# Performance work log

Hardware: AMD Instinct MI355X
Metric: run time of the kernel (lower is better)

Reference implementation:

```python
import jax, jax.numpy as jnp
import numpy as np

B, C, N, M, K = 1, 64, 65536, 65536, 16
H, O = 64, 128  # mlp hidden, out_channels


def setup_inputs() -> dict:
    key = jax.random.key(0)
    ks = jax.random.split(key, 8)
    return {
        "x": jax.random.normal(ks[0], (B, C, N), dtype=jnp.float32),
        "pos": jax.random.normal(ks[1], (B, 3, N), dtype=jnp.float32),
        "support_points": jax.random.normal(ks[2], (B, 3, M), dtype=jnp.float32),
        "W1": jax.random.normal(ks[3], (H, C + 3), dtype=jnp.float32) * 0.05,
        "b1": jax.random.normal(ks[4], (H,), dtype=jnp.float32) * 0.05,
        "W2": jax.random.normal(ks[5], (O, H), dtype=jnp.float32) * 0.05,
        "b2": jax.random.normal(ks[6], (O,), dtype=jnp.float32) * 0.05,
        "indices": jax.random.randint(ks[7], (B, M, K), 0, N, dtype=jnp.int64),
    }


def _gather_points(t, indices):
    # t: [B, C, N], indices: [B, M, K] -> [B, C, M, K]
    b, c, n = t.shape
    m, k = indices.shape[1], indices.shape[2]
    idx = indices.reshape(b, 1, m * k)  # broadcasts over channel dim
    return jnp.take_along_axis(t, idx, axis=2).reshape(b, c, m, k)


def reference(x, pos, support_points, W1, b1, W2, b2, indices):
    # gather neighbor features and positions: [B, C, M, K], [B, 3, M, K]
    feats = _gather_points(x, indices)
    pts = _gather_points(pos, indices) - support_points[:, :, :, None]
    h = jnp.concatenate([feats, pts], axis=1)  # [B, C+3, M, K]
    # shared per-point MLP (1x1 Conv2d == channel contraction)
    h = jnp.einsum("oc,bcmk->bomk", W1, h) + b1[None, :, None, None]
    h = jax.nn.relu(h)
    h = jnp.einsum("oc,bcmk->bomk", W2, h) + b2[None, :, None, None]
    # max-pool over neighborhood K -> [B, O, M]
    return jnp.max(h, axis=3)
```

## Files before the change

### kernel.cpp

```cpp
#include <hip/hip_runtime.h>
#include <hip/hip_bf16.h>

#define NPTS 65536
#define MPTS 65536

typedef __attribute__((ext_vector_type(8))) short bf16x8;
typedef __attribute__((ext_vector_type(4))) float f32x4;

__device__ __forceinline__ float bflo(unsigned int u){ union{unsigned int i; float f;} v; v.i = u<<16; return v.f; }
__device__ __forceinline__ float bfhi(unsigned int u){ union{unsigned int i; float f;} v; v.i = u & 0xffff0000u; return v.f; }
__device__ __forceinline__ unsigned short f2bf(float f){
  union{float f; unsigned int i;} v; v.f=f;
  unsigned int r = v.i + 0x7fffu + ((v.i>>16)&1u);
  return (unsigned short)(r>>16);
}
__device__ __forceinline__ unsigned int pk2f(float a, float b){
  float2 tf; tf.x = a; tf.y = b;
  union { __hip_bfloat162 h; unsigned int u; } c;
  c.h = __float22bfloat162_rn(tf);
  return c.u;
}

#define MFMA32(a,b,c) __builtin_amdgcn_mfma_f32_16x16x32_bf16((a),(b),(c),0,0,0)

__global__ __launch_bounds__(256) void pack_u(
    const float* __restrict__ x,
    const float* __restrict__ pos,
    const float* __restrict__ W1,
    const float* __restrict__ b1,
    const float* __restrict__ W2,
    unsigned short* __restrict__ U,
    unsigned short* __restrict__ W2F) {
  const int t = threadIdx.x;
  if (blockIdx.x >= 1024) {
    const int gg = (blockIdx.x - 1024) * 256 + t;
    if (gg < 1024) {
      const int g = gg >> 6, lane = gg & 63;
      const int q = lane >> 4, lr = lane & 15;
      const int kt = g >> 3, ot = g & 7;
      #pragma unroll
      for (int j = 0; j < 4; ++j)
        *(unsigned int*)&W2F[gg*8 + 2*j] =
            pk2f(W2[(ot*16 + lr)*64 + kt*32 + q*8 + 2*j],
                 W2[(ot*16 + lr)*64 + kt*32 + q*8 + 2*j + 1]);
    }
    return;
  }
  const int lane = t & 63, w = t >> 6, quad = lane >> 4, lr = lane & 15;
  const int n = blockIdx.x * 64 + w * 16 + lr;

  bf16x8 wa[2][4], wt[4];
  #pragma unroll
  for (int kt = 0; kt < 2; ++kt)
    #pragma unroll
    for (int nt = 0; nt < 4; ++nt) {
      const float* r = W1 + (size_t)(nt*16 + lr)*67 + kt*32 + quad*8;
      const float4 a = *(const float4*)r;
      const float4 b = *(const float4*)(r + 4);
      union { unsigned int d[4]; bf16x8 v; } mk;
      mk.d[0] = pk2f(a.x, a.y); mk.d[1] = pk2f(a.z, a.w);
      mk.d[2] = pk2f(b.x, b.y); mk.d[3] = pk2f(b.z, b.w);
      wa[kt][nt] = mk.v;
    }
  #pragma unroll
  for (int nt = 0; nt < 4; ++nt) {
    union { unsigned int d[4]; bf16x8 v; } mk;
    mk.d[0] = 0u; mk.d[1] = 0u; mk.d[2] = 0u; mk.d[3] = 0u;
    if (quad == 0) {
      const float* r = W1 + (size_t)(nt*16 + lr)*67 + 64;
      mk.d[0] = pk2f(r[0], r[1]);
      mk.d[1] = (unsigned int)f2bf(r[2]);
    }
    wt[nt] = mk.v;
  }

  const f32x4 fz = {0.f, 0.f, 0.f, 0.f};
  f32x4 acc[4] = {fz, fz, fz, fz};
  #pragma unroll
  for (int kt = 0; kt < 2; ++kt) {
    const float* xc = x + (size_t)(kt*32 + quad*8) * NPTS + n;
    union { unsigned int d[4]; bf16x8 v; } mk;
    #pragma unroll
    for (int i = 0; i < 4; ++i)
      mk.d[i] = pk2f(xc[(size_t)(2*i) * NPTS], xc[(size_t)(2*i + 1) * NPTS]);
    #pragma unroll
    for (int nt = 0; nt < 4; ++nt)
      acc[nt] = MFMA32(wa[kt][nt], mk.v, acc[nt]);
  }
  {
    union { unsigned int d[4]; bf16x8 v; } mk;
    mk.d[0] = pk2f(pos[n], pos[NPTS + n]);
    mk.d[1] = (unsigned int)f2bf(pos[2*NPTS + n]);
    mk.d[2] = 0u; mk.d[3] = 0u;
    #pragma unroll
    for (int nt = 0; nt < 4; ++nt)
      acc[nt] = MFMA32(wt[nt], mk.v, acc[nt]);
  }
  #pragma unroll
  for (int nt = 0; nt < 4; ++nt) {
    const float4 bb = *(const float4*)(b1 + nt*16 + quad*4);
    uint2 d;
    d.x = pk2f(acc[nt][0] + bb.x, acc[nt][1] + bb.y);
    d.y = pk2f(acc[nt][2] + bb.z, acc[nt][3] + bb.w);
    *(uint2*)(U + (size_t)n * 64 + nt*16 + quad*4) = d;
  }
}

__global__ __launch_bounds__(256, 3) void pointnet_reg(
    const unsigned short* __restrict__ U,
    const float* __restrict__ sup,
    const float* __restrict__ W1,
    const unsigned short* __restrict__ W2F,
    const float* __restrict__ b2,
    const int* __restrict__ indices,
    float* __restrict__ out) {
  const int t = threadIdx.x;
  const int lane = t & 63, w = t >> 6, quad = lane >> 4, lr = lane & 15;
  const int wbase = blockIdx.x * 32 + w * 8;

  int idx[8];
  #pragma unroll
  for (int pt = 0; pt < 8; ++pt) idx[pt] = indices[(wbase + pt)*16 + lr];

  uint4 ur[8][2];
  #pragma unroll
  for (int pt = 0; pt < 8; ++pt)
    #pragma unroll
    for (int kt = 0; kt < 2; ++kt)
      ur[pt][kt] = *(const uint4*)(U + (size_t)idx[pt]*64 + kt*32 + quad*8);

  bf16x8 ah[8][2];
  #pragma unroll
  for (int kt = 0; kt < 2; ++kt) {
    float w1p[8][3];
    #pragma unroll
    for (int j = 0; j < 8; ++j) {
      const float* r = W1 + (size_t)(kt*32 + quad*8 + j)*67 + 64;
      w1p[j][0] = r[0]; w1p[j][1] = r[1]; w1p[j][2] = r[2];
    }
    #pragma unroll
    for (int pt = 0; pt < 8; ++pt) {
      const float s0 = sup[wbase + pt];
      const float s1 = sup[MPTS + wbase + pt];
      const float s2 = sup[2*MPTS + wbase + pt];
      const unsigned int uu[4] = {ur[pt][kt].x, ur[pt][kt].y, ur[pt][kt].z, ur[pt][kt].w};
      union { unsigned int d[4]; bf16x8 v; } mk;
      #pragma unroll
      for (int i = 0; i < 4; ++i) {
        const float vl = w1p[2*i][0]*s0 + w1p[2*i][1]*s1 + w1p[2*i][2]*s2;
        const float vh = w1p[2*i+1][0]*s0 + w1p[2*i+1][1]*s1 + w1p[2*i+1][2]*s2;
        const float hl = fmaxf(bflo(uu[i]) - vl, 0.f);
        const float hh = fmaxf(bfhi(uu[i]) - vh, 0.f);
        mk.d[i] = pk2f(hl, hh);
      }
      ah[pt][kt] = mk.v;
    }
  }

  const f32x4 fz = {0.f, 0.f, 0.f, 0.f};
  #pragma unroll
  for (int ot = 0; ot < 8; ++ot) {
    const bf16x8 wb0 = ((const bf16x8*)W2F)[(0*8 + ot)*64 + lane];
    const bf16x8 wb1 = ((const bf16x8*)W2F)[(1*8 + ot)*64 + lane];
    float vm[8];
    #pragma unroll
    for (int pt = 0; pt < 8; ++pt) {
      f32x4 a2 = MFMA32(ah[pt][0], wb0, fz);
      a2 = MFMA32(ah[pt][1], wb1, a2);
      float v = fmaxf(fmaxf(a2[0], a2[1]), fmaxf(a2[2], a2[3]));
      v = fmaxf(v, __shfl_xor(v, 16));
      v = fmaxf(v, __shfl_xor(v, 32));
      vm[pt] = v;
    }
    const int o = ot*16 + lr;
    const float bb = b2[o];
    const float va = (quad & 1) ? ((quad & 2) ? vm[3] : vm[1])
                                : ((quad & 2) ? vm[2] : vm[0]);
    const float vb = (quad & 1) ? ((quad & 2) ? vm[7] : vm[5])
                                : ((quad & 2) ? vm[6] : vm[4]);
    out[(size_t)o * MPTS + wbase + quad] = va + bb;
    out[(size_t)o * MPTS + wbase + 4 + quad] = vb + bb;
  }
}

__global__ __launch_bounds__(256) void pointnet_fallback(
    const float* __restrict__ x, const float* __restrict__ pos,
    const float* __restrict__ sup,
    const float* __restrict__ W1, const float* __restrict__ b1,
    const float* __restrict__ W2, const float* __restrict__ b2,
    const int* __restrict__ indices, float* __restrict__ out) {
  __shared__ float sfeat[16][68];
  __shared__ float shid[16][64];
  __shared__ float smax[4][128];
  __shared__ int sidx[16];
  const int t = threadIdx.x;
  const int m = blockIdx.x;
  if (t < 16) sidx[t] = indices[m*16 + t];
  const float sup0 = sup[m], sup1 = sup[MPTS + m], sup2 = sup[2*MPTS + m];
  __syncthreads();
  for (int u = t; u < 16*17; u += 256) {
    const int k = u / 17, c4 = (u - k*17) * 4;
    const int idx = sidx[k];
    float4 wv;
    if (c4 < 64) {
      wv.x = x[(size_t)(c4+0)*NPTS + idx]; wv.y = x[(size_t)(c4+1)*NPTS + idx];
      wv.z = x[(size_t)(c4+2)*NPTS + idx]; wv.w = x[(size_t)(c4+3)*NPTS + idx];
    } else {
      wv.x = pos[idx] - sup0; wv.y = pos[NPTS + idx] - sup1;
      wv.z = pos[2*NPTS + idx] - sup2; wv.w = 0.f;
    }
    *(float4*)&sfeat[k][c4] = wv;
  }
  const int h = t & 63, kg = t >> 6;
  float w1r[68];
  #pragma unroll
  for (int c = 0; c < 67; ++c) w1r[c] = W1[h*67 + c];
  w1r[67] = 0.f;
  const float bias1 = b1[h];
  __syncthreads();
  #pragma unroll
  for (int j = 0; j < 4; ++j) {
    const int k = kg*4 + j;
    float a = bias1;
    const float4* rr = (const float4*)sfeat[k];
    #pragma unroll
    for (int qq = 0; qq < 17; ++qq) {
      const float4 v = rr[qq];
      a += w1r[qq*4+0]*v.x + w1r[qq*4+1]*v.y + w1r[qq*4+2]*v.z + w1r[qq*4+3]*v.w;
    }
    shid[k][h] = fmaxf(a, 0.f);
  }
  const int ow = t & 63;
  float w2a[64], w2b[64];
  #pragma unroll
  for (int hh = 0; hh < 64; ++hh) { w2a[hh] = W2[ow*64 + hh]; w2b[hh] = W2[(ow+64)*64 + hh]; }
  __syncthreads();
  float mxa = -3.0e38f, mxb = -3.0e38f;
  #pragma unroll
  for (int j = 0; j < 4; ++j) {
    const int k = kg*4 + j;
    const float4* hr = (const float4*)shid[k];
    float pa = 0.f, pb = 0.f;
    #pragma unroll
    for (int qq = 0; qq < 16; ++qq) {
      const float4 v = hr[qq];
      pa += w2a[qq*4+0]*v.x + w2a[qq*4+1]*v.y + w2a[qq*4+2]*v.z + w2a[qq*4+3]*v.w;
      pb += w2b[qq*4+0]*v.x + w2b[qq*4+1]*v.y + w2b[qq*4+2]*v.z + w2b[qq*4+3]*v.w;
    }
    mxa = fmaxf(mxa, pa); mxb = fmaxf(mxb, pb);
  }
  smax[kg][ow] = mxa; smax[kg][64 + ow] = mxb;
  __syncthreads();
  if (t < 128) {
    out[(size_t)t * MPTS + m] =
        fmaxf(fmaxf(smax[0][t], smax[1][t]), fmaxf(smax[2][t], smax[3][t])) + b2[t];
  }
}

extern "C" void kernel_launch(void* const* d_in, const int* in_sizes, int n_in,
                              void* d_out, int out_size, void* d_ws, size_t ws_size,
                              hipStream_t stream) {
  const float* x   = (const float*)d_in[0];
  const float* pos = (const float*)d_in[1];
  const float* sup = (const float*)d_in[2];
  const float* W1  = (const float*)d_in[3];
  const float* b1  = (const float*)d_in[4];
  const float* W2  = (const float*)d_in[5];
  const float* b2  = (const float*)d_in[6];
  const int* indices = (const int*)d_in[7];
  float* out = (float*)d_out;

  const size_t U_BYTES   = (size_t)NPTS * 64 * 2;
  const size_t W2F_BYTES = 16 * 64 * 8 * 2;
  if (ws_size >= U_BYTES + W2F_BYTES) {
    unsigned short* U   = (unsigned short*)d_ws;
    unsigned short* W2F = (unsigned short*)((char*)d_ws + U_BYTES);
    pack_u<<<NPTS/64 + 4, 256, 0, stream>>>(x, pos, W1, b1, W2, U, W2F);
    pointnet_reg<<<MPTS/32, 256, 0, stream>>>(U, sup, W1, W2F, b2, indices, out);
  } else {
    pointnet_fallback<<<MPTS, 256, 0, stream>>>(x, pos, sup, W1, b1, W2, b2, indices, out);
  }
}
```

Baseline: 136.9 us.

## Precompute per-support W1·support term into fp32 table and subtract in main kernel

Adds a pre-pass inside the pack kernel that computes, for each support point, the 64-wide product of the position columns of W1 with the support coordinates, stored as fp32 V. A new main kernel loads this row per support point and subtracts it from the gathered bf16 first-layer pre-activations before ReLU. This avoids recomputing the support-point contribution of W1 in the main kernel. In exchange it writes and reads an extra 16 MB fp32 workspace.

```diff
diff --git a/kernel.cpp b/kernel.cpp
--- a/kernel.cpp
+++ b/kernel.cpp
@@ -26,12 +26,32 @@
 __global__ __launch_bounds__(256) void pack_u(
     const float* __restrict__ x,
     const float* __restrict__ pos,
+    const float* __restrict__ sup,
     const float* __restrict__ W1,
     const float* __restrict__ b1,
     const float* __restrict__ W2,
     unsigned short* __restrict__ U,
-    unsigned short* __restrict__ W2F) {
+    unsigned short* __restrict__ W2F,
+    float* __restrict__ V) {
   const int t = threadIdx.x;
+  if (blockIdx.x >= 1028) {
+    const int m = (blockIdx.x - 1028) * 256 + t;
+    const float s0 = sup[m], s1 = sup[MPTS + m], s2 = sup[2*MPTS + m];
+    #pragma unroll
+    for (int cg = 0; cg < 16; ++cg) {
+      const float* r0 = W1 + (size_t)(cg*4 + 0)*67 + 64;
+      const float* r1 = W1 + (size_t)(cg*4 + 1)*67 + 64;
+      const float* r2 = W1 + (size_t)(cg*4 + 2)*67 + 64;
+      const float* r3 = W1 + (size_t)(cg*4 + 3)*67 + 64;
+      float4 o;
+      o.x = r0[0]*s0 + r0[1]*s1 + r0[2]*s2;
+      o.y = r1[0]*s0 + r1[1]*s1 + r1[2]*s2;
+      o.z = r2[0]*s0 + r2[1]*s1 + r2[2]*s2;
+      o.w = r3[0]*s0 + r3[1]*s1 + r3[2]*s2;
+      *(float4*)(V + (size_t)m*64 + cg*4) = o;
+    }
+    return;
+  }
   if (blockIdx.x >= 1024) {
     const int gg = (blockIdx.x - 1024) * 256 + t;
     if (gg < 1024) {
@@ -103,6 +123,77 @@
     d.x = pk2f(acc[nt][0] + bb.x, acc[nt][1] + bb.y);
     d.y = pk2f(acc[nt][2] + bb.z, acc[nt][3] + bb.w);
     *(uint2*)(U + (size_t)n * 64 + nt*16 + quad*4) = d;
+  }
+}
+
+__global__ __launch_bounds__(256, 3) void pointnet_reg2(
+    const unsigned short* __restrict__ U,
+    const float* __restrict__ V,
+    const unsigned short* __restrict__ W2F,
+    const float* __restrict__ b2,
+    const int* __restrict__ indices,
+    float* __restrict__ out) {
+  const int t = threadIdx.x;
+  const int lane = t & 63, w = t >> 6, quad = lane >> 4, lr = lane & 15;
+  const int wbase = blockIdx.x * 32 + w * 8;
+
+  int idx[8];
+  #pragma unroll
+  for (int pt = 0; pt < 8; ++pt) idx[pt] = indices[(wbase + pt)*16 + lr];
+
+  uint4 ur[8][2];
+  #pragma unroll
+  for (int pt = 0; pt < 8; ++pt)
+    #pragma unroll
+    for (int kt = 0; kt < 2; ++kt)
+      ur[pt][kt] = *(const uint4*)(U + (size_t)idx[pt]*64 + kt*32 + quad*8);
+
+  bf16x8 ah[8][2];
+  #pragma unroll
+  for (int pt = 0; pt < 8; ++pt) {
+    const float* vr = V + (size_t)(wbase + pt)*64 + quad*8;
+    float vv[16];
+    *(float4*)&vv[0]  = *(const float4*)(vr);
+    *(float4*)&vv[4]  = *(const float4*)(vr + 4);
+    *(float4*)&vv[8]  = *(const float4*)(vr + 32);
+    *(float4*)&vv[12] = *(const float4*)(vr + 36);
+    #pragma unroll
+    for (int kt = 0; kt < 2; ++kt) {
+      const unsigned int uu[4] = {ur[pt][kt].x, ur[pt][kt].y, ur[pt][kt].z, ur[pt][kt].w};
+      union { unsigned int d[4]; bf16x8 v; } mk;
+      #pragma unroll
+      for (int i = 0; i < 4; ++i) {
+        const float lo = bflo(uu[i]) - vv[kt*8 + 2*i];
+        const float hi = bfhi(uu[i]) - vv[kt*8 + 2*i + 1];
+        mk.d[i] = pk2f(fmaxf(lo, 0.f), fmaxf(hi, 0.f));
+      }
+      ah[pt][kt] = mk.v;
+    }
+  }
+
+  const f32x4 fz = {0.f, 0.f, 0.f, 0.f};
+  #pragma unroll
+  for (int ot = 0; ot < 8; ++ot) {
+    const bf16x8 wb0 = ((const bf16x8*)W2F)[(0*8 + ot)*64 + lane];
+    const bf16x8 wb1 = ((const bf16x8*)W2F)[(1*8 + ot)*64 + lane];
+    float vm[8];
+    #pragma unroll
+    for (int pt = 0; pt < 8; ++pt) {
+      f32x4 a2 = MFMA32(ah[pt][0], wb0, fz);
+      a2 = MFMA32(ah[pt][1], wb1, a2);
+      float v = fmaxf(fmaxf(a2[0], a2[1]), fmaxf(a2[2], a2[3]));
+      v = fmaxf(v, __int_as_float(__builtin_amdgcn_ds_swizzle(__float_as_int(v), 0x401F)));
+      v = fmaxf(v, __shfl_xor(v, 32));
+      vm[pt] = v;
+    }
+    const int o = ot*16 + lr;
+    const float bb = b2[o];
+    const float va = (quad & 1) ? ((quad & 2) ? vm[3] : vm[1])
+                                : ((quad & 2) ? vm[2] : vm[0]);
+    const float vb = (quad & 1) ? ((quad & 2) ? vm[7] : vm[5])
+                                : ((quad & 2) ? vm[6] : vm[4]);
+    out[(size_t)o * MPTS + wbase + quad] = va + bb;
+    out[(size_t)o * MPTS + wbase + 4 + quad] = vb + bb;
   }
 }
 
@@ -272,10 +363,17 @@
 
   const size_t U_BYTES   = (size_t)NPTS * 64 * 2;
   const size_t W2F_BYTES = 16 * 64 * 8 * 2;
-  if (ws_size >= U_BYTES + W2F_BYTES) {
+  const size_t V_BYTES   = (size_t)MPTS * 64 * 4;
+  if (ws_size >= U_BYTES + W2F_BYTES + V_BYTES) {
     unsigned short* U   = (unsigned short*)d_ws;
     unsigned short* W2F = (unsigned short*)((char*)d_ws + U_BYTES);
-    pack_u<<<NPTS/64 + 4, 256, 0, stream>>>(x, pos, W1, b1, W2, U, W2F);
+    float* V            = (float*)((char*)d_ws + U_BYTES + W2F_BYTES);
+    pack_u<<<1028 + 256, 256, 0, stream>>>(x, pos, sup, W1, b1, W2, U, W2F, V);
+    pointnet_reg2<<<MPTS/32, 256, 0, stream>>>(U, V, W2F, b2, indices, out);
+  } else if (ws_size >= U_BYTES + W2F_BYTES) {
+    unsigned short* U   = (unsigned short*)d_ws;
+    unsigned short* W2F = (unsigned short*)((char*)d_ws + U_BYTES);
+    pack_u<<<1028, 256, 0, stream>>>(x, pos, sup, W1, b1, W2, U, W2F, nullptr);
     pointnet_reg<<<MPTS/32, 256, 0, stream>>>(U, sup, W1, W2F, b2, indices, out);
   } else {
     pointnet_fallback<<<MPTS, 256, 0, stream>>>(x, pos, sup, W1, b1, W2, b2, indices, out);
```

Result: slower. 139.9 us (+2.2%).
